# Performance work log

Hardware: AMD Instinct MI355X
Metric: run time of the kernel (lower is better)

## Reference

```python
import jax, jax.numpy as jnp
import numpy as np
from functools import partial

# CUBA LIF/LI constants (mock-mode software integration, hxtorch conventions)
DT = 1e-6
TAU_MEM_INV = 1.0 / 6e-6   # dt*tau_mem_inv = 1/6 per-step membrane coupling
TAU_SYN_INV = 1.0 / 6e-6   # dt*tau_syn_inv = 1/6 per-step synaptic decay
ALPHA = 50.0               # SuperSpike surrogate steepness
V_TH = 1.0                 # threshold; leak = reset = 0


@partial(jax.custom_vjp, nondiff_argnums=(1,))
def spike_fn(x, alpha):
    # Heaviside forward, SuperSpike surrogate backward.
    return (x > 0.0).astype(x.dtype)

def _spike_fwd(x, alpha):
    return spike_fn(x, alpha), x

def _spike_bwd(alpha, x, g):
    return (g / (alpha * jnp.abs(x) + 1.0) ** 2,)

spike_fn.defvjp(_spike_fwd, _spike_bwd)


def cuba_lif(inp):
    """CUBA LIF integration over time. inp: [T, B, N] synaptic input; returns spikes [T, B, N]."""
    B, N = inp.shape[1], inp.shape[2]
    v0 = jnp.zeros((B, N), inp.dtype)
    i0 = jnp.zeros((B, N), inp.dtype)

    def step(carry, x):
        v, i = carry
        v = v + DT * TAU_MEM_INV * (-v + i)          # membrane update (leak=0)
        i = i * (1.0 - DT * TAU_SYN_INV) + x          # synaptic current decay + input
        z = spike_fn(v - V_TH, ALPHA)                 # spike
        v = (1.0 - jax.lax.stop_gradient(z)) * v      # reset to 0 (detached spike)
        return (v, i), z

    _, z = jax.lax.scan(step, (v0, i0), inp)
    return z


def cuba_li(inp):
    """CUBA LI (non-spiking readout) integration. inp: [T, B, N]; returns membrane trace [T, B, N]."""
    B, N = inp.shape[1], inp.shape[2]
    v0 = jnp.zeros((B, N), inp.dtype)
    i0 = jnp.zeros((B, N), inp.dtype)

    def step(carry, x):
        v, i = carry
        v = v + DT * TAU_MEM_INV * (-v + i)
        i = i * (1.0 - DT * TAU_SYN_INV) + x
        return (v, i), v

    _, v = jax.lax.scan(step, (v0, i0), inp)
    return v


def setup_inputs() -> dict:
    key = jax.random.key(0)
    k1, k2, k3 = jax.random.split(key, 3)
    T, B, N_IN, N_HID, N_OUT = 256, 128, 784, 512, 128
    spikes = (jax.random.uniform(k1, (T, B, N_IN)) < 0.1).astype(jnp.float32)
    w_hidden = 0.2 * jax.random.normal(k2, (N_HID, N_IN), dtype=jnp.float32)
    w_out = 0.2 * jax.random.normal(k3, (N_OUT, N_HID), dtype=jnp.float32)
    return {"spikes": spikes, "w_hidden": w_hidden, "w_out": w_out}


def reference(spikes, w_hidden, w_out):
    # input_repetitions=1 -> repeat is a no-op. Synapses have no bias.
    c_h = jnp.einsum('tbi,hi->tbh', spikes, w_hidden)   # [T, B, n_hidden]
    s_h = cuba_lif(c_h)                                  # hidden spikes
    c_o = jnp.einsum('tbh,oh->tbo', s_h, w_out)          # [T, B, n_out]
    return cuba_li(c_o)                                  # readout membrane trace (v_cadc)
```

## Files before the change

kernel.cpp:

```cpp
#include <hip/hip_runtime.h>

typedef _Float16 f16;
typedef _Float16 f16x8 __attribute__((ext_vector_type(8)));
typedef float f32x4 __attribute__((ext_vector_type(4)));

#define GLOBAL_AS __attribute__((address_space(1)))
#define LDS_AS __attribute__((address_space(3)))

__device__ __forceinline__ void async16(const void* g, void* l) {
  __builtin_amdgcn_global_load_lds((const GLOBAL_AS unsigned int*)g,
                                   (LDS_AS unsigned int*)l, 16, 0, 0);
}

__global__ __launch_bounds__(256) void conv_all(const float* __restrict__ s,
                                                const float* __restrict__ wh,
                                                const float* __restrict__ wo,
                                                f16* __restrict__ a16,
                                                f16* __restrict__ w2h,
                                                f16* __restrict__ w2o) {
  if (blockIdx.x < 12800) {
    int idx = blockIdx.x * 256 + threadIdx.x;
    int m = idx / 100;
    int g = idx - m * 100;
    f16x8 h = {};
    if (g < 98) {
      const float4* p = (const float4*)(s + (size_t)m * 784 + g * 8);
      float4 x = p[0];
      float4 y = p[1];
      h[0] = (f16)x.x; h[1] = (f16)x.y; h[2] = (f16)x.z; h[3] = (f16)x.w;
      h[4] = (f16)y.x; h[5] = (f16)y.y; h[6] = (f16)y.z; h[7] = (f16)y.w;
    }
    *(f16x8*)(a16 + (size_t)m * 800 + g * 8) = h;
  } else {
    int idx = (blockIdx.x - 12800) * 256 + threadIdx.x;
    if (idx < 819200) {
      int h = idx / 1600;
      int c = idx - h * 1600;
      f16 o = (f16)0.f;
      if (c < 784) {
        o = (f16)wh[h * 784 + c];
      } else if (c >= 800 && c < 1584) {
        float x = wh[h * 784 + (c - 800)];
        f16 hi = (f16)x;
        o = (f16)((x - (float)hi) * 2048.0f);
      }
      w2h[idx] = o;
    } else if (idx < 819200 + 65536) {
      int j = idx - 819200;
      w2o[j] = (f16)wo[j];
    }
  }
}

template <typename OUT, int N_LD, int A_STRIDE, int B_STRIDE, int NCH64,
          bool TAIL32, int B_OFF_LO, int KSPLIT_SPAN, bool XCD_SWZ>
__global__ __launch_bounds__(256, 2) void gemm_f16(const f16* __restrict__ A,
                                                   const f16* __restrict__ B,
                                                   OUT* __restrict__ C) {
  constexpr bool HAS_LO = (B_OFF_LO > 0);
  __shared__ __align__(16) f16 lds_a[128 * 64];
  __shared__ __align__(16) f16 lds_bh[128 * 64];
  __shared__ __align__(16) f16 lds_bl[HAS_LO ? 128 * 64 : 8];
  const int t = threadIdx.x;
  const int lane = t & 63;
  const int wave = t >> 6;
  int bx, by;
  if (XCD_SWZ) {
    const int b = blockIdx.x;
    by = (b & 7) + 8 * (b >> 5);
    bx = (b >> 3) & 3;
  } else {
    bx = blockIdx.x;
    by = blockIdx.y;
  }
  const int m0 = by * 128;
  const int n0 = KSPLIT_SPAN ? 0 : bx * 128;
  const int kb = KSPLIT_SPAN ? bx * KSPLIT_SPAN : 0;
  OUT* Cp = KSPLIT_SPAN ? C + (size_t)bx * 32768 * N_LD : C;
  const int wm = (wave >> 1) * 64;
  const int wn = (wave & 1) * 64;
  const int row = lane & 15;
  const int quad = lane >> 4;

  f32x4 acch[4][4] = {};
  f32x4 accl[HAS_LO ? 4 : 1][4] = {};

  for (int c = 0; c < NCH64; ++c) {
    const int k0 = kb + c * 64;
#pragma unroll
    for (int s = 0; s < 4; ++s) {
      const int j = t + s * 256;
      const int r = j >> 3;
      const int g = (j & 7) ^ (r & 7);
      async16(A + (m0 + r) * A_STRIDE + k0 + g * 8, &lds_a[j * 8]);
      async16(B + (n0 + r) * B_STRIDE + k0 + g * 8, &lds_bh[j * 8]);
      if (HAS_LO)
        async16(B + (n0 + r) * B_STRIDE + B_OFF_LO + k0 + g * 8, &lds_bl[j * 8]);
    }
    __syncthreads();
#pragma unroll
    for (int ks = 0; ks < 2; ++ks) {
      f16x8 af[4], bh[4], bl[4];
#pragma unroll
      for (int tm = 0; tm < 4; ++tm) {
        const int ra = wm + tm * 16 + row;
        const int p = (ks * 4 + quad) ^ (ra & 7);
        af[tm] = *(const f16x8*)&lds_a[ra * 64 + p * 8];
      }
#pragma unroll
      for (int tn = 0; tn < 4; ++tn) {
        const int rb = wn + tn * 16 + row;
        const int p = (ks * 4 + quad) ^ (rb & 7);
        bh[tn] = *(const f16x8*)&lds_bh[rb * 64 + p * 8];
        if (HAS_LO) bl[tn] = *(const f16x8*)&lds_bl[rb * 64 + p * 8];
      }
#pragma unroll
      for (int tm = 0; tm < 4; ++tm)
#pragma unroll
        for (int tn = 0; tn < 4; ++tn) {
          acch[tm][tn] =
              __builtin_amdgcn_mfma_f32_16x16x32_f16(af[tm], bh[tn], acch[tm][tn], 0, 0, 0);
          if (HAS_LO)
            accl[tm][tn] =
                __builtin_amdgcn_mfma_f32_16x16x32_f16(af[tm], bl[tn], accl[tm][tn], 0, 0, 0);
        }
    }
    __syncthreads();
  }

  if (TAIL32) {
    const int k0 = kb + NCH64 * 64;
#pragma unroll
    for (int s = 0; s < 2; ++s) {
      const int j = t + s * 256;
      const int r = j >> 2;
      const int g = (j & 3) ^ (r & 3);
      async16(A + (m0 + r) * A_STRIDE + k0 + g * 8, &lds_a[j * 8]);
      async16(B + (n0 + r) * B_STRIDE + k0 + g * 8, &lds_bh[j * 8]);
      if (HAS_LO)
        async16(B + (n0 + r) * B_STRIDE + B_OFF_LO + k0 + g * 8, &lds_bl[j * 8]);
    }
    __syncthreads();
    f16x8 af[4], bh[4], bl[4];
#pragma unroll
    for (int tm = 0; tm < 4; ++tm) {
      const int ra = wm + tm * 16 + row;
      const int p = quad ^ (ra & 3);
      af[tm] = *(const f16x8*)&lds_a[ra * 32 + p * 8];
    }
#pragma unroll
    for (int tn = 0; tn < 4; ++tn) {
      const int rb = wn + tn * 16 + row;
      const int p = quad ^ (rb & 3);
      bh[tn] = *(const f16x8*)&lds_bh[rb * 32 + p * 8];
      if (HAS_LO) bl[tn] = *(const f16x8*)&lds_bl[rb * 32 + p * 8];
    }
#pragma unroll
    for (int tm = 0; tm < 4; ++tm)
#pragma unroll
      for (int tn = 0; tn < 4; ++tn) {
        acch[tm][tn] =
            __builtin_amdgcn_mfma_f32_16x16x32_f16(af[tm], bh[tn], acch[tm][tn], 0, 0, 0);
        if (HAS_LO)
          accl[tm][tn] =
              __builtin_amdgcn_mfma_f32_16x16x32_f16(af[tm], bl[tn], accl[tm][tn], 0, 0, 0);
      }
  }

#pragma unroll
  for (int tm = 0; tm < 4; ++tm)
#pragma unroll
    for (int tn = 0; tn < 4; ++tn)
#pragma unroll
      for (int r = 0; r < 4; ++r) {
        const int mm = m0 + wm + tm * 16 + quad * 4 + r;
        const int nn = n0 + wn + tn * 16 + row;
        float val = acch[tm][tn][r];
        if (HAS_LO) val += 4.8828125e-4f * accl[tm][tn][r];
        Cp[(size_t)mm * N_LD + nn] = (OUT)val;
      }
}

__global__ __launch_bounds__(256) void lif_scan(const f16* __restrict__ ch,
                                                f16* __restrict__ sh) {
  const int n = blockIdx.x * 256 + threadIdx.x;
  f16 xa[32], xb[32];
#pragma unroll
  for (int j = 0; j < 32; ++j) xa[j] = ch[j * 65536 + n];
  float v = 0.f, cur = 0.f;
  for (int c = 0; c < 8; ++c) {
    const int nc = (c + 1) & 7;
#pragma unroll
    for (int j = 0; j < 32; ++j) xb[j] = ch[(nc * 32 + j) * 65536 + n];
#pragma unroll
    for (int j = 0; j < 32; ++j) {
      const int t = c * 32 + j;
      float x = (float)xa[j];
      v = v + 0.16666667f * (cur - v);
      cur = 0.8333333f * cur + x;
      bool z = v > 1.0f;
      sh[t * 65536 + n] = z ? (f16)1.f : (f16)0.f;
      v = z ? 0.f : v;
    }
#pragma unroll
    for (int j = 0; j < 32; ++j) xa[j] = xb[j];
  }
}

__global__ __launch_bounds__(256) void li_scan_seg(const f16* __restrict__ coA,
                                                   const f16* __restrict__ coB,
                                                   float* __restrict__ out) {
  const int tid = blockIdx.x * 256 + threadIdx.x;
  const int n = tid & 16383;
  const int seg = tid >> 14;
  const int t0 = seg * 64;
  float v = 0.f, cur = 0.f;
  float xa[8], xb[8];
  if (seg) {
    const int w0 = t0 - 64;
#pragma unroll
    for (int j = 0; j < 8; ++j)
      xa[j] = (float)coA[(w0 + j) * 16384 + n] + (float)coB[(w0 + j) * 16384 + n];
    for (int c = 0; c < 8; ++c) {
      const int nb = w0 + (c + 1) * 8;
#pragma unroll
      for (int j = 0; j < 8; ++j)
        xb[j] = (float)coA[(nb + j) * 16384 + n] + (float)coB[(nb + j) * 16384 + n];
#pragma unroll
      for (int j = 0; j < 8; ++j) {
        v = v + 0.16666667f * (cur - v);
        cur = 0.8333333f * cur + xa[j];
      }
#pragma unroll
      for (int j = 0; j < 8; ++j) xa[j] = xb[j];
    }
  } else {
#pragma unroll
    for (int j = 0; j < 8; ++j)
      xa[j] = (float)coA[j * 16384 + n] + (float)coB[j * 16384 + n];
  }
  for (int c = 0; c < 8; ++c) {
    if (c < 7) {
      const int nb = t0 + (c + 1) * 8;
#pragma unroll
      for (int j = 0; j < 8; ++j)
        xb[j] = (float)coA[(nb + j) * 16384 + n] + (float)coB[(nb + j) * 16384 + n];
    }
#pragma unroll
    for (int j = 0; j < 8; ++j) {
      const int t = t0 + c * 8 + j;
      v = v + 0.16666667f * (cur - v);
      cur = 0.8333333f * cur + xa[j];
      out[t * 16384 + n] = v;
    }
#pragma unroll
    for (int j = 0; j < 8; ++j) xa[j] = xb[j];
  }
}

extern "C" void kernel_launch(void* const* d_in, const int* in_sizes, int n_in,
                              void* d_out, int out_size, void* d_ws, size_t ws_size,
                              hipStream_t stream) {
  const float* spikes = (const float*)d_in[0];
  const float* w_hidden = (const float*)d_in[1];
  const float* w_out = (const float*)d_in[2];
  float* out = (float*)d_out;

  char* ws = (char*)d_ws;
  f16* A16 = (f16*)ws;
  f16* coA = (f16*)ws;
  f16* coB = (f16*)(ws + 8388608);
  f16* w2h = (f16*)(ws + 52428800);
  f16* c_h = (f16*)(ws + 52428800 + 1638400);
  f16* s_h = (f16*)(ws + 52428800 + 1638400 + 33554432);
  f16* w2o = (f16*)(ws + 52428800 + 1638400 + 33554432 + 33554432);

  conv_all<<<16256, 256, 0, stream>>>(spikes, w_hidden, w_out, A16, w2h, w2o);

  gemm_f16<f16, 512, 800, 1600, 12, true, 800, 0, true>
      <<<1024, 256, 0, stream>>>(A16, w2h, c_h);

  lif_scan<<<256, 256, 0, stream>>>(c_h, s_h);

  gemm_f16<f16, 128, 512, 512, 4, false, 0, 256, false>
      <<<dim3(2, 256), 256, 0, stream>>>(s_h, w2o, coA);

  li_scan_seg<<<256, 256, 0, stream>>>(coA, coB, out);
}
```

Measured before the change: 239.0 us.

## Fuse LIF scan, readout GEMM and LI scan into one per-batch kernel

Replaces the separate LIF scan, second GEMM and LI scan kernels with a single kernel per batch row. Hidden spikes stay in LDS and feed MFMA against w_out fragments held in registers (converted from fp32 in-kernel), and the LI readout integrates directly from LDS. This removes the large global round trips for hidden spikes and readout currents, along with two launches. In exchange it runs only 128 blocks with block-wide syncs and a serial 128-thread readout per chunk, which may limit parallelism.

```diff
diff --git a/kernel.cpp b/kernel.cpp
--- a/kernel.cpp
+++ b/kernel.cpp
@@ -14,10 +14,8 @@
 
 __global__ __launch_bounds__(256) void conv_all(const float* __restrict__ s,
                                                 const float* __restrict__ wh,
-                                                const float* __restrict__ wo,
                                                 f16* __restrict__ a16,
-                                                f16* __restrict__ w2h,
-                                                f16* __restrict__ w2o) {
+                                                f16* __restrict__ w2h) {
   if (blockIdx.x < 12800) {
     int idx = blockIdx.x * 256 + threadIdx.x;
     int m = idx / 100;
@@ -45,9 +43,6 @@
         o = (f16)((x - (float)hi) * 2048.0f);
       }
       w2h[idx] = o;
-    } else if (idx < 819200 + 65536) {
-      int j = idx - 819200;
-      w2o[j] = (f16)wo[j];
     }
   }
 }
@@ -181,80 +176,87 @@
       }
 }
 
-__global__ __launch_bounds__(256) void lif_scan(const f16* __restrict__ ch,
-                                                f16* __restrict__ sh) {
-  const int n = blockIdx.x * 256 + threadIdx.x;
+__global__ __launch_bounds__(512, 2) void fused_bgl(const f16* __restrict__ ch,
+                                                    const float* __restrict__ wo,
+                                                    float* __restrict__ out) {
+  const int b = blockIdx.x;
+  const int tid = threadIdx.x;
+  const int lane = tid & 63;
+  const int wave = tid >> 6;
+  const int trow = lane & 15;
+  const int quad = lane >> 4;
+
+  __shared__ __align__(16) f16 s_lds[32 * 512];
+  __shared__ __align__(16) float co_lds[32][132];
+
+  f16x8 bfrag[16];
+  {
+    const float* wp = wo + (wave * 16 + trow) * 512 + quad * 8;
+#pragma unroll
+    for (int ks = 0; ks < 16; ++ks) {
+      const float4* p = (const float4*)(wp + ks * 32);
+      float4 x = p[0];
+      float4 y = p[1];
+      f16x8 hh;
+      hh[0] = (f16)x.x; hh[1] = (f16)x.y; hh[2] = (f16)x.z; hh[3] = (f16)x.w;
+      hh[4] = (f16)y.x; hh[5] = (f16)y.y; hh[6] = (f16)y.z; hh[7] = (f16)y.w;
+      bfrag[ks] = hh;
+    }
+  }
+
+  const int h = tid;
+  float v = 0.f, cur = 0.f;
+  float lv = 0.f, lcur = 0.f;
+
   f16 xa[32], xb[32];
 #pragma unroll
-  for (int j = 0; j < 32; ++j) xa[j] = ch[j * 65536 + n];
-  float v = 0.f, cur = 0.f;
+  for (int j = 0; j < 32; ++j) xa[j] = ch[((size_t)(j * 128 + b)) * 512 + h];
+
   for (int c = 0; c < 8; ++c) {
-    const int nc = (c + 1) & 7;
-#pragma unroll
-    for (int j = 0; j < 32; ++j) xb[j] = ch[(nc * 32 + j) * 65536 + n];
+    if (c < 7) {
+#pragma unroll
+      for (int j = 0; j < 32; ++j)
+        xb[j] = ch[((size_t)(((c + 1) * 32 + j) * 128 + b)) * 512 + h];
+    }
 #pragma unroll
     for (int j = 0; j < 32; ++j) {
-      const int t = c * 32 + j;
       float x = (float)xa[j];
       v = v + 0.16666667f * (cur - v);
       cur = 0.8333333f * cur + x;
       bool z = v > 1.0f;
-      sh[t * 65536 + n] = z ? (f16)1.f : (f16)0.f;
       v = z ? 0.f : v;
+      s_lds[j * 512 + (((h >> 3) ^ (j & 7)) << 3) + (h & 7)] = z ? (f16)1.f : (f16)0.f;
     }
 #pragma unroll
     for (int j = 0; j < 32; ++j) xa[j] = xb[j];
-  }
-}
-
-__global__ __launch_bounds__(256) void li_scan_seg(const f16* __restrict__ coA,
-                                                   const f16* __restrict__ coB,
-                                                   float* __restrict__ out) {
-  const int tid = blockIdx.x * 256 + threadIdx.x;
-  const int n = tid & 16383;
-  const int seg = tid >> 14;
-  const int t0 = seg * 64;
-  float v = 0.f, cur = 0.f;
-  float xa[8], xb[8];
-  if (seg) {
-    const int w0 = t0 - 64;
-#pragma unroll
-    for (int j = 0; j < 8; ++j)
-      xa[j] = (float)coA[(w0 + j) * 16384 + n] + (float)coB[(w0 + j) * 16384 + n];
-    for (int c = 0; c < 8; ++c) {
-      const int nb = w0 + (c + 1) * 8;
-#pragma unroll
-      for (int j = 0; j < 8; ++j)
-        xb[j] = (float)coA[(nb + j) * 16384 + n] + (float)coB[(nb + j) * 16384 + n];
-#pragma unroll
-      for (int j = 0; j < 8; ++j) {
-        v = v + 0.16666667f * (cur - v);
-        cur = 0.8333333f * cur + xa[j];
-      }
-#pragma unroll
-      for (int j = 0; j < 8; ++j) xa[j] = xb[j];
-    }
-  } else {
-#pragma unroll
-    for (int j = 0; j < 8; ++j)
-      xa[j] = (float)coA[j * 16384 + n] + (float)coB[j * 16384 + n];
-  }
-  for (int c = 0; c < 8; ++c) {
-    if (c < 7) {
-      const int nb = t0 + (c + 1) * 8;
-#pragma unroll
-      for (int j = 0; j < 8; ++j)
-        xb[j] = (float)coA[(nb + j) * 16384 + n] + (float)coB[(nb + j) * 16384 + n];
-    }
-#pragma unroll
-    for (int j = 0; j < 8; ++j) {
-      const int t = t0 + c * 8 + j;
-      v = v + 0.16666667f * (cur - v);
-      cur = 0.8333333f * cur + xa[j];
-      out[t * 16384 + n] = v;
-    }
-#pragma unroll
-    for (int j = 0; j < 8; ++j) xa[j] = xb[j];
+    __syncthreads();
+
+    f32x4 acc0 = {};
+    f32x4 acc1 = {};
+#pragma unroll
+    for (int ks = 0; ks < 16; ++ks) {
+      const int G = ks * 4 + quad;
+      f16x8 a0 = *(const f16x8*)&s_lds[trow * 512 + ((G ^ (trow & 7)) << 3)];
+      f16x8 a1 = *(const f16x8*)&s_lds[(16 + trow) * 512 + ((G ^ (trow & 7)) << 3)];
+      acc0 = __builtin_amdgcn_mfma_f32_16x16x32_f16(a0, bfrag[ks], acc0, 0, 0, 0);
+      acc1 = __builtin_amdgcn_mfma_f32_16x16x32_f16(a1, bfrag[ks], acc1, 0, 0, 0);
+    }
+#pragma unroll
+    for (int r = 0; r < 4; ++r) {
+      co_lds[quad * 4 + r][wave * 16 + trow] = acc0[r];
+      co_lds[16 + quad * 4 + r][wave * 16 + trow] = acc1[r];
+    }
+    __syncthreads();
+
+    if (tid < 128) {
+#pragma unroll
+      for (int j = 0; j < 32; ++j) {
+        float x = co_lds[j][tid];
+        lv = lv + 0.16666667f * (lcur - lv);
+        lcur = 0.8333333f * lcur + x;
+        out[((size_t)((c * 32 + j) * 128 + b)) * 128 + tid] = lv;
+      }
+    }
   }
 }
 
@@ -268,22 +270,13 @@
 
   char* ws = (char*)d_ws;
   f16* A16 = (f16*)ws;
-  f16* coA = (f16*)ws;
-  f16* coB = (f16*)(ws + 8388608);
   f16* w2h = (f16*)(ws + 52428800);
   f16* c_h = (f16*)(ws + 52428800 + 1638400);
-  f16* s_h = (f16*)(ws + 52428800 + 1638400 + 33554432);
-  f16* w2o = (f16*)(ws + 52428800 + 1638400 + 33554432 + 33554432);
-
-  conv_all<<<16256, 256, 0, stream>>>(spikes, w_hidden, w_out, A16, w2h, w2o);
+
+  conv_all<<<16000, 256, 0, stream>>>(spikes, w_hidden, A16, w2h);
 
   gemm_f16<f16, 512, 800, 1600, 12, true, 800, 0, true>
       <<<1024, 256, 0, stream>>>(A16, w2h, c_h);
 
-  lif_scan<<<256, 256, 0, stream>>>(c_h, s_h);
-
-  gemm_f16<f16, 128, 512, 512, 4, false, 0, 256, false>
-      <<<dim3(2, 256), 256, 0, stream>>>(s_h, w2o, coA);
-
-  li_scan_seg<<<256, 256, 0, stream>>>(coA, coB, out);
-}
+  fused_bgl<<<128, 512, 0, stream>>>(c_h, w_out, out);
+}
```

Result: no change. 239.3 us (median of 2 runs) (+0.1%).
